# Optimization experiments

Hardware: AMD Instinct MI355X
Metric: run time of the kernel (lower is better)

## Reference

```python
import jax, jax.numpy as jnp
import numpy as np

K = 3; PAD = 1; CIN = 64; COUT = 64; B = 4; H = 128; W = 128


def setup_inputs() -> dict:
    key = jax.random.key(0)
    k1, k2, k3 = jax.random.split(key, 3)
    x = jax.random.normal(k1, (B, CIN, H, W), dtype=jnp.float32)
    # offset-predicting conv: [2*K*K, Cin, K, K]; small init -> sub-pixel offsets
    w_off = jax.random.normal(k2, (2 * K * K, CIN, K, K), dtype=jnp.float32) * 0.01
    b_off = jnp.zeros((2 * K * K,), dtype=jnp.float32)
    # deformable conv weight (bias=False): [Cout, Cin, K, K]
    w_def = jax.random.normal(k3, (COUT, CIN, K, K), dtype=jnp.float32) * 0.05
    return {"x": x, "w_off": w_off, "b_off": b_off, "w_def": w_def}


def _deform_conv(x, w_off, b_off, w_def):
    Bb, Cin, Hh, Ww = x.shape
    KK = K * K
    # 1) predict offsets with a regular 3x3 conv (stride 1, pad 1)
    off = jax.lax.conv_general_dilated(
        x, w_off, window_strides=(1, 1), padding=[(PAD, PAD), (PAD, PAD)],
        dimension_numbers=("NCHW", "OIHW", "NCHW"))
    off = off + b_off[None, :, None, None]          # [B, 2*KK, H, W]
    off = off.reshape(Bb, KK, 2, Hh, Ww)            # torchvision layout: (dy, dx) per tap
    dy, dx = off[:, :, 0], off[:, :, 1]             # [B, KK, H, W]

    # 2) sampling coordinates: p = p0 + p_k + offset
    ky = (jnp.arange(KK) // K).astype(x.dtype)
    kx = (jnp.arange(KK) % K).astype(x.dtype)
    hh = jnp.arange(Hh, dtype=x.dtype)
    ww = jnp.arange(Ww, dtype=x.dtype)
    py = hh[None, None, :, None] - PAD + ky[None, :, None, None] + dy   # [B,KK,H,W]
    px = ww[None, None, None, :] - PAD + kx[None, :, None, None] + dx

    # 3) bilinear sampling with zero padding outside the image
    y0f = jnp.floor(py); x0f = jnp.floor(px)
    fy = py - y0f; fx = px - x0f
    y0 = y0f.astype(jnp.int32); x0 = x0f.astype(jnp.int32)
    x_flat = x.reshape(Bb, Cin, Hh * Ww)

    def gather(yi, xi):
        valid = (yi >= 0) & (yi < Hh) & (xi >= 0) & (xi < Ww)
        idx = jnp.clip(yi, 0, Hh - 1) * Ww + jnp.clip(xi, 0, Ww - 1)     # [B,KK,H,W]
        g = jax.vmap(lambda xf, ix: xf[:, ix.reshape(-1)])(x_flat, idx)  # [B,Cin,KK*H*W]
        return g.reshape(Bb, Cin, KK, Hh, Ww) * valid[:, None].astype(x.dtype)

    sampled = (gather(y0, x0)         * ((1 - fy) * (1 - fx))[:, None]
             + gather(y0, x0 + 1)     * ((1 - fy) * fx)[:, None]
             + gather(y0 + 1, x0)     * (fy * (1 - fx))[:, None]
             + gather(y0 + 1, x0 + 1) * (fy * fx)[:, None])               # [B,Cin,KK,H,W]

    # 4) convolution accumulation over (Cin, kernel taps)
    return jnp.einsum('bckhw,ock->bohw', sampled, w_def.reshape(COUT, Cin, KK))


def reference(x, w_off, b_off, w_def):
    return _deform_conv(x, w_off, b_off, w_def)
```

## Files before the change

### kernel.cpp

```cpp
#include <hip/hip_runtime.h>
#include <hip/hip_fp16.h>

#define Bn   4
#define CINc 64
#define COUTc 64
#define Hn   128
#define Wn   128
#define HW   (Hn * Wn)
#define KKc  9
#define NOFF 18

typedef short bf16x8 __attribute__((ext_vector_type(8)));
typedef float f32x4  __attribute__((ext_vector_type(4)));
typedef float f32x2  __attribute__((ext_vector_type(2)));

__device__ inline unsigned short f2bf(float f) {
    unsigned int u = __float_as_uint(f);
    return (unsigned short)((u + 0x7fffu + ((u >> 16) & 1u)) >> 16);
}

__device__ inline void dma16(const void* g, void* l) {
#if __has_builtin(__builtin_amdgcn_global_load_lds)
    __builtin_amdgcn_global_load_lds(
        (__attribute__((address_space(1))) void*)(g),
        (__attribute__((address_space(3))) void*)(l), 16, 0, 0);
#else
    *(uint4*)l = *(const uint4*)g;
#endif
}

__global__ __launch_bounds__(256) void prep_all(
        const float* __restrict__ x, unsigned short* __restrict__ xt,
        const float* __restrict__ w_off, const float* __restrict__ w_def,
        unsigned short* __restrict__ wkb_sw, unsigned short* __restrict__ wob_sw) {
    int gb = blockIdx.x;
    int t  = threadIdx.x;
    if (gb < 1024) {
        __shared__ float s[64][65];
        int half = gb & 1;
        int h    = (gb >> 1) & 127;
        int b    = gb >> 8;
        int w0   = half * 64;
        int w = t & 63, cg = t >> 6;

        const float* xb = x + (size_t)b * CINc * HW + (size_t)h * Wn + w0 + w;
        #pragma unroll
        for (int i = 0; i < 16; ++i) {
            int c = cg * 16 + i;
            s[c][w] = xb[(size_t)c * HW];
        }
        __syncthreads();

        int cpair = t & 31, pxg = t >> 5;
        unsigned* xtp = (unsigned*)xt;
        #pragma unroll
        for (int i = 0; i < 8; ++i) {
            int px = pxg * 8 + i;
            float v0 = s[cpair * 2][px], v1 = s[cpair * 2 + 1][px];
            unsigned d = (unsigned)f2bf(v0) | ((unsigned)f2bf(v1) << 16);
            xtp[(((size_t)(b * Hn + h) * Wn) + w0 + px) * 32 + cpair] = d;
        }
        return;
    }
    int idx = (gb - 1024) * 256 + t;
    if (idx < 36864) {
        int j = idx & 7, l = (idx >> 3) & 63, s = idx >> 9;
        int k = s >> 3, kc = (s >> 2) & 1, ot = s & 3;
        int l15 = l & 15, quad = l >> 4;
        int o = ot * 16 + l15, c = kc * 32 + quad * 8 + j;
        wkb_sw[idx] = f2bf(w_def[((size_t)o * 64 + c) * 9 + k]);
    }
    int i2 = idx - 36864;
    if (i2 >= 0 && i2 < 18432) {
        int j = i2 & 7, l = (i2 >> 3) & 63, s = i2 >> 9;
        int tt = s >> 2, kc = (s >> 1) & 1, mt = s & 1;
        int l15 = l & 15, quad = l >> 4;
        int m = mt * 16 + l15, c = kc * 32 + quad * 8 + j;
        unsigned short v = 0;
        if (m < NOFF) v = f2bf(w_off[((size_t)m * 64 + c) * 9 + tt]);
        wob_sw[i2] = v;
    }
}


#define BFBUILD(C, kc, BF, W0, W1, W2, W3)                                   \
    do {                                                                     \
        const unsigned* t0 = (const unsigned*)&(C)[(kc) * 4 + 0];            \
        const unsigned* t1 = (const unsigned*)&(C)[(kc) * 4 + 1];            \
        const unsigned* b0 = (const unsigned*)&(C)[(kc) * 4 + 2];            \
        const unsigned* b1 = (const unsigned*)&(C)[(kc) * 4 + 3];            \
        _Pragma("unroll")                                                    \
        for (int jd = 0; jd < 4; ++jd) {                                     \
            f32x2 t0p = {__uint_as_float(t0[jd] << 16),                      \
                         __uint_as_float(t0[jd] & 0xFFFF0000u)};             \
            f32x2 t1p = {__uint_as_float(t1[jd] << 16),                      \
                         __uint_as_float(t1[jd] & 0xFFFF0000u)};             \
            f32x2 b0p = {__uint_as_float(b0[jd] << 16),                      \
                         __uint_as_float(b0[jd] & 0xFFFF0000u)};             \
            f32x2 b1p = {__uint_as_float(b1[jd] << 16),                      \
                         __uint_as_float(b1[jd] & 0xFFFF0000u)};             \
            f32x2 vv = t0p * (W0) + t1p * (W1) + b0p * (W2) + b1p * (W3);    \
            unsigned pk;                                                     \
            asm("v_cvt_pk_bf16_f32 %0, %1, %2"                               \
                : "=v"(pk) : "v"(vv.x), "v"(vv.y));                          \
            (BF).u[jd] = pk;                                                 \
        }                                                                    \
    } while (0)

#define TAP(k, SOFF)                                                         \
    do {                                                                     \
        const uint4* C = R[(k) & 1];                                         \
        union { unsigned u; __half2 hv; } c01, c23;                          \
        c01.u = pw01[(k)]; c23.u = pw23[(k)];                                \
        float W0 = __low2float(c01.hv), W1 = __high2float(c01.hv);           \
        float W2 = __low2float(c23.hv), W3 = __high2float(c23.hv);           \
        union { bf16x8 v; unsigned u[4]; } bfa, bfb;                         \
        BFBUILD(C, 0, bfa, W0, W1, W2, W3);                                  \
        BFBUILD(C, 1, bfb, W0, W1, W2, W3);                                  \
        _Pragma("unroll")                                                    \
        for (int ot = 0; ot < 4; ++ot) {                                     \
            bf16x8 af0 = s_w[(((k) * 2 + 0) * 4 + ot + (SOFF)) * 64 + lane]; \
            acc[ot] = __builtin_amdgcn_mfma_f32_16x16x32_bf16(               \
                af0, bfa.v, acc[ot], 0, 0, 0);                               \
            bf16x8 af1 = s_w[(((k) * 2 + 1) * 4 + ot + (SOFF)) * 64 + lane]; \
            acc[ot] = __builtin_amdgcn_mfma_f32_16x16x32_bf16(               \
                af1, bfb.v, acc[ot], 0, 0, 0);                               \
        }                                                                    \
    } while (0)

__global__ __launch_bounds__(512, 4) void fused_deform_v13(
        const unsigned short* __restrict__ xt,
        const unsigned short* __restrict__ wob_sw,
        const unsigned short* __restrict__ wkb_sw,
        const float* __restrict__ b_off, float* __restrict__ out) {
    __shared__ bf16x8 s_w[40 * 64];

    int gid  = blockIdx.x;
    int xcd  = gid & 7;
    int j    = gid >> 3;
    int hh   = j & 15;
    int b    = j >> 4;
    int h    = xcd * 16 + hh;
    int tid  = threadIdx.x;
    int lane = tid & 63;
    int wave = __builtin_amdgcn_readfirstlane(tid >> 6);
    int l15  = lane & 15;
    int quad = lane >> 4;
    int p    = wave * 16 + l15;

    #pragma unroll
    for (int i = 0; i < 5; ++i) {
        int seg = i * 8 + wave;
        if (seg < 36) {
            int ebase = seg * 64;
            dma16((const uint4*)wob_sw + ebase + lane,
                  (char*)s_w + (size_t)ebase * 16);
        }
    }

    uint4 L[9][2];
    unsigned msk[9];
    const unsigned short* xtb = xt + (size_t)b * HW * 64;
    #pragma unroll
    for (int t9 = 0; t9 < 9; ++t9) {
        int ty = t9 / 3, tx = t9 % 3;
        int y  = h - 1 + ty;
        int xg = p - 1 + tx;
        bool v = (y >= 0) && (y < Hn) && (xg >= 0) && (xg < Wn);
        msk[t9] = v ? 0xFFFFFFFFu : 0u;
        int yc = min(max(y, 0), Hn - 1);
        int xc = min(max(xg, 0), Wn - 1);
        size_t base = ((size_t)yc * Wn + xc) * 64;
        L[t9][0] = *(const uint4*)(xtb + base + quad * 8);
        L[t9][1] = *(const uint4*)(xtb + base + 32 + quad * 8);
    }
    __syncthreads();

    f32x4 oa0 = (f32x4){0.f, 0.f, 0.f, 0.f};
    f32x4 oa1 = (f32x4){0.f, 0.f, 0.f, 0.f};
    #pragma unroll
    for (int t9 = 0; t9 < 9; ++t9) {
        unsigned m = msk[t9];
        #pragma unroll
        for (int kc = 0; kc < 2; ++kc) {
            union { bf16x8 v; uint4 u; } bf;
            bf.u = L[t9][kc];
            bf.u.x &= m; bf.u.y &= m; bf.u.z &= m; bf.u.w &= m;
            bf16x8 a0 = s_w[((t9 * 2 + kc) * 2 + 0) * 64 + lane];
            bf16x8 a1 = s_w[((t9 * 2 + kc) * 2 + 1) * 64 + lane];
            oa0 = __builtin_amdgcn_mfma_f32_16x16x32_bf16(a0, bf.v, oa0, 0, 0, 0);
            oa1 = __builtin_amdgcn_mfma_f32_16x16x32_bf16(a1, bf.v, oa1, 0, 0, 0);
        }
    }

    unsigned my_ad[3]  = {0, 0, 0};
    unsigned my_w01[3] = {0, 0, 0};
    unsigned my_w23[3] = {0, 0, 0};
    auto phase1 = [&](int k, float dy, float dx, int slot) {
        float py  = (float)(h - 1 + k / 3) + dy;
        float pxf = (float)(p - 1 + k % 3) + dx;
        float y0f = floorf(py), x0f = floorf(pxf);
        float fy = py - y0f, fx = pxf - x0f;
        int y0 = (int)y0f, x0 = (int)x0f;
        bool vy0 = (y0 >= 0) & (y0 < Hn);
        bool vy1 = (y0 + 1 >= 0) & (y0 + 1 < Hn);
        bool vx0 = (x0 >= 0) & (x0 < Wn);
        bool vx1 = (x0 + 1 >= 0) & (x0 + 1 < Wn);
        float wy0 = vy0 ? 1.f - fy : 0.f;
        float wy1 = vy1 ? fy : 0.f;
        float wx0 = vx0 ? 1.f - fx : 0.f;
        float wx1 = vx1 ? fx : 0.f;
        int xc = min(max(x0, 0), Wn - 2);
        bool sel0 = (min(max(x0, 0), Wn - 1) != xc);
        bool sel1 = ((min(max(x0 + 1, 0), Wn - 1) - xc) == 1);
        float Wa = (sel0 ? 0.f : wx0) + (sel1 ? 0.f : wx1);
        float Wb = (sel0 ? wx0 : 0.f) + (sel1 ? wx1 : 0.f);
        int yc0 = min(max(y0, 0), Hn - 1), yc1 = min(max(y0 + 1, 0), Hn - 1);
        union { __half2 hv; unsigned u; } c01, c23;
        c01.hv = __floats2half2_rn(wy0 * Wa, wy0 * Wb);
        c23.hv = __floats2half2_rn(wy1 * Wa, wy1 * Wb);
        my_ad[slot]  = (unsigned)yc0 | ((unsigned)yc1 << 8) | ((unsigned)xc << 16);
        my_w01[slot] = c01.u;
        my_w23[slot] = c23.u;
    };
    int kb = quad * 2;
    phase1(kb,     oa0[0] + b_off[4 * quad],     oa0[1] + b_off[4 * quad + 1], 0);
    phase1(kb + 1, oa0[2] + b_off[4 * quad + 2], oa0[3] + b_off[4 * quad + 3], 1);
    if (quad == 0)
        phase1(8, oa1[0] + b_off[16], oa1[1] + b_off[17], 2);
    __syncthreads();

    #pragma unroll
    for (int i = 0; i < 4; ++i) {
        int seg = i * 8 + wave;
        dma16((const uint4*)wkb_sw + (size_t)seg * 64 + lane,
              (char*)s_w + (size_t)seg * 1024);
    }

    unsigned at[KKc], ab[KKc];
    unsigned pw01[KKc], pw23[KKc];
    #pragma unroll
    for (int k = 0; k < KKc; ++k) {
        int src  = (k < 8) ? ((k >> 1) * 16 + l15) : l15;
        int slot = (k < 8) ? (k & 1) : 2;
        unsigned ad  = (unsigned)__shfl((int)my_ad[slot],  src, 64);
        pw01[k] = (unsigned)__shfl((int)my_w01[slot], src, 64);
        pw23[k] = (unsigned)__shfl((int)my_w23[slot], src, 64);
        int xc = (int)(ad >> 16);
        at[k] = (unsigned)(((ad & 255u) * Wn + xc) * 64);
        ab[k] = (unsigned)((((ad >> 8) & 255u) * Wn + xc) * 64);
    }
    __syncthreads();

    f32x4 acc[4];
    #pragma unroll
    for (int ot = 0; ot < 4; ++ot) acc[ot] = (f32x4){0.f, 0.f, 0.f, 0.f};

    uint4 R[2][8];
    int co0 = quad * 8, co1 = 32 + quad * 8;

    #define FETCH(kk, st)                                            \
        do {                                                         \
            R[st][0] = *(const uint4*)(xtb + at[kk] + co0);          \
            R[st][1] = *(const uint4*)(xtb + at[kk] + 64 + co0);     \
            R[st][2] = *(const uint4*)(xtb + ab[kk] + co0);          \
            R[st][3] = *(const uint4*)(xtb + ab[kk] + 64 + co0);     \
            R[st][4] = *(const uint4*)(xtb + at[kk] + co1);          \
            R[st][5] = *(const uint4*)(xtb + at[kk] + 64 + co1);     \
            R[st][6] = *(const uint4*)(xtb + ab[kk] + co1);          \
            R[st][7] = *(const uint4*)(xtb + ab[kk] + 64 + co1);     \
        } while (0)

    FETCH(0, 0);
    FETCH(1, 1); TAP(0, 0);
    FETCH(2, 0); TAP(1, 0);
    FETCH(3, 1); TAP(2, 0);
    FETCH(4, 0); TAP(3, 0);
    __syncthreads();

    #pragma unroll
    for (int i = 0; i < 5; ++i) {
        int seg = i * 8 + wave;
        dma16((const uint4*)wkb_sw + (size_t)(32 + seg) * 64 + lane,
              (char*)s_w + (size_t)seg * 1024);
    }

    union { bf16x8 v; unsigned u[4]; } bf40, bf41;
    {
        const uint4* C = R[0];
        union { unsigned u; __half2 hv; } c01, c23;
        c01.u = pw01[4]; c23.u = pw23[4];
        float W0 = __low2float(c01.hv), W1 = __high2float(c01.hv);
        float W2 = __low2float(c23.hv), W3 = __high2float(c23.hv);
        BFBUILD(C, 0, bf40, W0, W1, W2, W3);
        BFBUILD(C, 1, bf41, W0, W1, W2, W3);
    }
    FETCH(5, 1);
    __syncthreads();

    #pragma unroll
    for (int ot = 0; ot < 4; ++ot) {
        bf16x8 af0 = s_w[(0 + ot) * 64 + lane];
        acc[ot] = __builtin_amdgcn_mfma_f32_16x16x32_bf16(af0, bf40.v, acc[ot], 0, 0, 0);
        bf16x8 af1 = s_w[(4 + ot) * 64 + lane];
        acc[ot] = __builtin_amdgcn_mfma_f32_16x16x32_bf16(af1, bf41.v, acc[ot], 0, 0, 0);
    }

    FETCH(6, 0); TAP(5, -32);
    FETCH(7, 1); TAP(6, -32);
    FETCH(8, 0); TAP(7, -32);
    TAP(8, -32);
    #undef FETCH

    #pragma unroll
    for (int ot = 0; ot < 4; ++ot)
        #pragma unroll
        for (int r = 0; r < 4; ++r) {
            int o = ot * 16 + quad * 4 + r;
            out[(((size_t)b * COUTc + o) * Hn + h) * Wn + p] = acc[ot][r];
        }
}

extern "C" void kernel_launch(void* const* d_in, const int* in_sizes, int n_in,
                              void* d_out, int out_size, void* d_ws, size_t ws_size,
                              hipStream_t stream) {
    const float* x     = (const float*)d_in[0];
    const float* w_off = (const float*)d_in[1];
    const float* b_off = (const float*)d_in[2];
    const float* w_def = (const float*)d_in[3];
    float* out = (float*)d_out;

    char* ws = (char*)d_ws;
    unsigned short* xt = (unsigned short*)ws;
    ws += (size_t)Bn * HW * CINc * sizeof(unsigned short);
    unsigned short* wkb_sw = (unsigned short*)ws;
    ws += 36864 * sizeof(unsigned short);
    unsigned short* wob_sw = (unsigned short*)ws;

    prep_all<<<1024 + 216, 256, 0, stream>>>(x, xt, w_off, w_def, wkb_sw, wob_sw);
    fused_deform_v13<<<Bn * Hn, 512, 0, stream>>>(xt, wob_sw, wkb_sw, b_off, out);
}
```

Before: 115.5 us.

## Split fused deform kernel into offset kernel and half-row gather/MFMA kernel

Splits the fused kernel into two launches. The first predicts the offsets and writes per-pixel, per-tap sampling records (address and fp16 bilinear weights) to workspace. The second reads those records back and does the gather and MFMA accumulation, using 256-thread blocks over half a row so it launches twice as many blocks. This aims to raise parallelism and occupancy for the gather/MFMA phase. The cost is an extra launch and a round trip of about 7 MB of records through global memory.

```diff
diff --git a/kernel.cpp b/kernel.cpp
--- a/kernel.cpp
+++ b/kernel.cpp
@@ -128,12 +128,29 @@
         }                                                                    \
     } while (0)
 
-__global__ __launch_bounds__(512, 4) void fused_deform_v13(
+#define FETCH(kk, st)                                                \
+    do {                                                             \
+        unsigned ad_ = ad[kk];                                       \
+        unsigned xc_ = ad_ >> 16;                                    \
+        unsigned at_ = (((ad_ & 255u) << 7) + xc_) << 6;             \
+        unsigned ab_ = ((((ad_ >> 8) & 255u) << 7) + xc_) << 6;      \
+        R[st][0] = *(const uint4*)(xtb + at_ + co0);                 \
+        R[st][1] = *(const uint4*)(xtb + at_ + 64 + co0);            \
+        R[st][2] = *(const uint4*)(xtb + ab_ + co0);                 \
+        R[st][3] = *(const uint4*)(xtb + ab_ + 64 + co0);            \
+        R[st][4] = *(const uint4*)(xtb + at_ + co1);                 \
+        R[st][5] = *(const uint4*)(xtb + at_ + 64 + co1);            \
+        R[st][6] = *(const uint4*)(xtb + ab_ + co1);                 \
+        R[st][7] = *(const uint4*)(xtb + ab_ + 64 + co1);            \
+    } while (0)
+
+__global__ __launch_bounds__(512, 4) void offs_k(
         const unsigned short* __restrict__ xt,
         const unsigned short* __restrict__ wob_sw,
-        const unsigned short* __restrict__ wkb_sw,
-        const float* __restrict__ b_off, float* __restrict__ out) {
-    __shared__ bf16x8 s_w[40 * 64];
+        const float* __restrict__ b_off,
+        unsigned* __restrict__ rec_ad, unsigned* __restrict__ rec_w01,
+        unsigned* __restrict__ rec_w23) {
+    __shared__ bf16x8 s_w[36 * 64];
 
     int gid  = blockIdx.x;
     int xcd  = gid & 7;
@@ -228,27 +245,58 @@
     phase1(kb + 1, oa0[2] + b_off[4 * quad + 2], oa0[3] + b_off[4 * quad + 3], 1);
     if (quad == 0)
         phase1(8, oa1[0] + b_off[16], oa1[1] + b_off[17], 2);
-    __syncthreads();
-
-    #pragma unroll
-    for (int i = 0; i < 4; ++i) {
-        int seg = i * 8 + wave;
+
+    int rb = ((b * Hn + h) * KKc) * Wn + p;
+    rec_ad [rb + kb * Wn]       = my_ad[0];
+    rec_w01[rb + kb * Wn]       = my_w01[0];
+    rec_w23[rb + kb * Wn]       = my_w23[0];
+    rec_ad [rb + (kb + 1) * Wn] = my_ad[1];
+    rec_w01[rb + (kb + 1) * Wn] = my_w01[1];
+    rec_w23[rb + (kb + 1) * Wn] = my_w23[1];
+    if (quad == 0) {
+        rec_ad [rb + 8 * Wn] = my_ad[2];
+        rec_w01[rb + 8 * Wn] = my_w01[2];
+        rec_w23[rb + 8 * Wn] = my_w23[2];
+    }
+}
+
+__global__ __launch_bounds__(256, 4) void gmain(
+        const unsigned short* __restrict__ xt,
+        const unsigned short* __restrict__ wkb_sw,
+        const unsigned* __restrict__ rec_ad, const unsigned* __restrict__ rec_w01,
+        const unsigned* __restrict__ rec_w23, float* __restrict__ out) {
+    __shared__ bf16x8 s_w[40 * 64];
+
+    int gid  = blockIdx.x;
+    int xcd  = gid & 7;
+    int t2   = gid >> 3;
+    int wh   = t2 & 1;
+    int jj   = t2 >> 1;
+    int hh   = jj & 15;
+    int b    = jj >> 4;
+    int h    = xcd * 16 + hh;
+    int tid  = threadIdx.x;
+    int lane = tid & 63;
+    int wave = __builtin_amdgcn_readfirstlane(tid >> 6);
+    int l15  = lane & 15;
+    int quad = lane >> 4;
+    int p    = wh * 64 + wave * 16 + l15;
+
+    #pragma unroll
+    for (int i = 0; i < 8; ++i) {
+        int seg = i * 4 + wave;
         dma16((const uint4*)wkb_sw + (size_t)seg * 64 + lane,
               (char*)s_w + (size_t)seg * 1024);
     }
 
-    unsigned at[KKc], ab[KKc];
-    unsigned pw01[KKc], pw23[KKc];
+    const unsigned short* xtb = xt + (size_t)b * HW * 64;
+    unsigned ad[KKc], pw01[KKc], pw23[KKc];
+    int rb = ((b * Hn + h) * KKc) * Wn + p;
     #pragma unroll
     for (int k = 0; k < KKc; ++k) {
-        int src  = (k < 8) ? ((k >> 1) * 16 + l15) : l15;
-        int slot = (k < 8) ? (k & 1) : 2;
-        unsigned ad  = (unsigned)__shfl((int)my_ad[slot],  src, 64);
-        pw01[k] = (unsigned)__shfl((int)my_w01[slot], src, 64);
-        pw23[k] = (unsigned)__shfl((int)my_w23[slot], src, 64);
-        int xc = (int)(ad >> 16);
-        at[k] = (unsigned)(((ad & 255u) * Wn + xc) * 64);
-        ab[k] = (unsigned)((((ad >> 8) & 255u) * Wn + xc) * 64);
+        ad[k]   = rec_ad [rb + k * Wn];
+        pw01[k] = rec_w01[rb + k * Wn];
+        pw23[k] = rec_w23[rb + k * Wn];
     }
     __syncthreads();
 
@@ -258,18 +306,6 @@
 
     uint4 R[2][8];
     int co0 = quad * 8, co1 = 32 + quad * 8;
-
-    #define FETCH(kk, st)                                            \
-        do {                                                         \
-            R[st][0] = *(const uint4*)(xtb + at[kk] + co0);          \
-            R[st][1] = *(const uint4*)(xtb + at[kk] + 64 + co0);     \
-            R[st][2] = *(const uint4*)(xtb + ab[kk] + co0);          \
-            R[st][3] = *(const uint4*)(xtb + ab[kk] + 64 + co0);     \
-            R[st][4] = *(const uint4*)(xtb + at[kk] + co1);          \
-            R[st][5] = *(const uint4*)(xtb + at[kk] + 64 + co1);     \
-            R[st][6] = *(const uint4*)(xtb + ab[kk] + co1);          \
-            R[st][7] = *(const uint4*)(xtb + ab[kk] + 64 + co1);     \
-        } while (0)
 
     FETCH(0, 0);
     FETCH(1, 1); TAP(0, 0);
@@ -279,8 +315,8 @@
     __syncthreads();
 
     #pragma unroll
-    for (int i = 0; i < 5; ++i) {
-        int seg = i * 8 + wave;
+    for (int i = 0; i < 10; ++i) {
+        int seg = i * 4 + wave;
         dma16((const uint4*)wkb_sw + (size_t)(32 + seg) * 64 + lane,
               (char*)s_w + (size_t)seg * 1024);
     }
@@ -310,7 +346,6 @@
     FETCH(7, 1); TAP(6, -32);
     FETCH(8, 0); TAP(7, -32);
     TAP(8, -32);
-    #undef FETCH
 
     #pragma unroll
     for (int ot = 0; ot < 4; ++ot)
@@ -336,7 +371,14 @@
     unsigned short* wkb_sw = (unsigned short*)ws;
     ws += 36864 * sizeof(unsigned short);
     unsigned short* wob_sw = (unsigned short*)ws;
+    ws += 36864;
+    unsigned* rec_ad = (unsigned*)ws;
+    ws += (size_t)Bn * Hn * KKc * Wn * 4;
+    unsigned* rec_w01 = (unsigned*)ws;
+    ws += (size_t)Bn * Hn * KKc * Wn * 4;
+    unsigned* rec_w23 = (unsigned*)ws;
 
     prep_all<<<1024 + 216, 256, 0, stream>>>(x, xt, w_off, w_def, wkb_sw, wob_sw);
-    fused_deform_v13<<<Bn * Hn, 512, 0, stream>>>(xt, wob_sw, wkb_sw, b_off, out);
-}
+    offs_k<<<Bn * Hn, 512, 0, stream>>>(xt, wob_sw, b_off, rec_ad, rec_w01, rec_w23);
+    gmain<<<Bn * Hn * 2, 256, 0, stream>>>(xt, wkb_sw, rec_ad, rec_w01, rec_w23, out);
+}
```

New measurement: 120.9 us. 4.7% more time.

## Split each row across two 256-thread blocks and vectorize the prep transpose loads

Applied to the files above, without the earlier changes.

The fused kernel now launches twice as many blocks with 256 threads each, each block covering half an image row. Shared memory for the weight tiles shrinks to 36 segments, so the deform-weight staging is restructured into three DMA phases, with tap 8 handled in its own phase. The per-tap address arithmetic is recomputed inside FETCH from packed coordinates rather than held in precomputed arrays, which lowers register pressure. The prep transpose now reads x with float4 loads. The aim is better occupancy and load balance, at the cost of more block launches, extra barriers and every block reloading the offset weights.

```diff
diff --git a/kernel.cpp b/kernel.cpp
--- a/kernel.cpp
+++ b/kernel.cpp
@@ -41,13 +41,17 @@
         int h    = (gb >> 1) & 127;
         int b    = gb >> 8;
         int w0   = half * 64;
-        int w = t & 63, cg = t >> 6;
-
-        const float* xb = x + (size_t)b * CINc * HW + (size_t)h * Wn + w0 + w;
+
+        const float* xb = x + (size_t)b * CINc * HW + (size_t)h * Wn + w0;
+        int c0 = t >> 4, wq = (t & 15) * 4;
         #pragma unroll
-        for (int i = 0; i < 16; ++i) {
-            int c = cg * 16 + i;
-            s[c][w] = xb[(size_t)c * HW];
+        for (int i = 0; i < 4; ++i) {
+            int c = c0 + i * 16;
+            float4 v = *(const float4*)(xb + (size_t)c * HW + wq);
+            s[c][wq]     = v.x;
+            s[c][wq + 1] = v.y;
+            s[c][wq + 2] = v.z;
+            s[c][wq + 3] = v.w;
         }
         __syncthreads();
 
@@ -128,16 +132,34 @@
         }                                                                    \
     } while (0)
 
-__global__ __launch_bounds__(512, 4) void fused_deform_v13(
+#define FETCH(kk, st)                                                \
+    do {                                                             \
+        unsigned ad_ = ad[kk];                                       \
+        unsigned xc_ = ad_ >> 16;                                    \
+        unsigned at_ = (((ad_ & 255u) << 7) + xc_) << 6;             \
+        unsigned ab_ = ((((ad_ >> 8) & 255u) << 7) + xc_) << 6;      \
+        R[st][0] = *(const uint4*)(xtb + at_ + co0);                 \
+        R[st][1] = *(const uint4*)(xtb + at_ + 64 + co0);            \
+        R[st][2] = *(const uint4*)(xtb + ab_ + co0);                 \
+        R[st][3] = *(const uint4*)(xtb + ab_ + 64 + co0);            \
+        R[st][4] = *(const uint4*)(xtb + at_ + co1);                 \
+        R[st][5] = *(const uint4*)(xtb + at_ + 64 + co1);            \
+        R[st][6] = *(const uint4*)(xtb + ab_ + co1);                 \
+        R[st][7] = *(const uint4*)(xtb + ab_ + 64 + co1);            \
+    } while (0)
+
+__global__ __launch_bounds__(256, 4) void fused_deform_v18(
         const unsigned short* __restrict__ xt,
         const unsigned short* __restrict__ wob_sw,
         const unsigned short* __restrict__ wkb_sw,
         const float* __restrict__ b_off, float* __restrict__ out) {
-    __shared__ bf16x8 s_w[40 * 64];
+    __shared__ bf16x8 s_w[36 * 64];
 
     int gid  = blockIdx.x;
     int xcd  = gid & 7;
-    int j    = gid >> 3;
+    int r    = gid >> 3;
+    int wh   = r & 1;
+    int j    = r >> 1;
     int hh   = j & 15;
     int b    = j >> 4;
     int h    = xcd * 16 + hh;
@@ -146,16 +168,14 @@
     int wave = __builtin_amdgcn_readfirstlane(tid >> 6);
     int l15  = lane & 15;
     int quad = lane >> 4;
-    int p    = wave * 16 + l15;
-
-    #pragma unroll
-    for (int i = 0; i < 5; ++i) {
-        int seg = i * 8 + wave;
-        if (seg < 36) {
-            int ebase = seg * 64;
-            dma16((const uint4*)wob_sw + ebase + lane,
-                  (char*)s_w + (size_t)ebase * 16);
-        }
+    int p    = wh * 64 + wave * 16 + l15;
+
+    #pragma unroll
+    for (int i = 0; i < 9; ++i) {
+        int seg = i * 4 + wave;
+        int ebase = seg * 64;
+        dma16((const uint4*)wob_sw + ebase + lane,
+              (char*)s_w + (size_t)ebase * 16);
     }
 
     uint4 L[9][2];
@@ -231,24 +251,20 @@
     __syncthreads();
 
     #pragma unroll
-    for (int i = 0; i < 4; ++i) {
-        int seg = i * 8 + wave;
+    for (int i = 0; i < 8; ++i) {
+        int seg = i * 4 + wave;
         dma16((const uint4*)wkb_sw + (size_t)seg * 64 + lane,
               (char*)s_w + (size_t)seg * 1024);
     }
 
-    unsigned at[KKc], ab[KKc];
-    unsigned pw01[KKc], pw23[KKc];
+    unsigned ad[KKc], pw01[KKc], pw23[KKc];
     #pragma unroll
     for (int k = 0; k < KKc; ++k) {
         int src  = (k < 8) ? ((k >> 1) * 16 + l15) : l15;
         int slot = (k < 8) ? (k & 1) : 2;
-        unsigned ad  = (unsigned)__shfl((int)my_ad[slot],  src, 64);
+        ad[k]   = (unsigned)__shfl((int)my_ad[slot],  src, 64);
         pw01[k] = (unsigned)__shfl((int)my_w01[slot], src, 64);
         pw23[k] = (unsigned)__shfl((int)my_w23[slot], src, 64);
-        int xc = (int)(ad >> 16);
-        at[k] = (unsigned)(((ad & 255u) * Wn + xc) * 64);
-        ab[k] = (unsigned)((((ad >> 8) & 255u) * Wn + xc) * 64);
     }
     __syncthreads();
 
@@ -258,18 +274,6 @@
 
     uint4 R[2][8];
     int co0 = quad * 8, co1 = 32 + quad * 8;
-
-    #define FETCH(kk, st)                                            \
-        do {                                                         \
-            R[st][0] = *(const uint4*)(xtb + at[kk] + co0);          \
-            R[st][1] = *(const uint4*)(xtb + at[kk] + 64 + co0);     \
-            R[st][2] = *(const uint4*)(xtb + ab[kk] + co0);          \
-            R[st][3] = *(const uint4*)(xtb + ab[kk] + 64 + co0);     \
-            R[st][4] = *(const uint4*)(xtb + at[kk] + co1);          \
-            R[st][5] = *(const uint4*)(xtb + at[kk] + 64 + co1);     \
-            R[st][6] = *(const uint4*)(xtb + ab[kk] + co1);          \
-            R[st][7] = *(const uint4*)(xtb + ab[kk] + 64 + co1);     \
-        } while (0)
 
     FETCH(0, 0);
     FETCH(1, 1); TAP(0, 0);
@@ -279,8 +283,8 @@
     __syncthreads();
 
     #pragma unroll
-    for (int i = 0; i < 5; ++i) {
-        int seg = i * 8 + wave;
+    for (int i = 0; i < 8; ++i) {
+        int seg = i * 4 + wave;
         dma16((const uint4*)wkb_sw + (size_t)(32 + seg) * 64 + lane,
               (char*)s_w + (size_t)seg * 1024);
     }
@@ -309,15 +313,41 @@
     FETCH(6, 0); TAP(5, -32);
     FETCH(7, 1); TAP(6, -32);
     FETCH(8, 0); TAP(7, -32);
-    TAP(8, -32);
-    #undef FETCH
+    __syncthreads();
+
+    #pragma unroll
+    for (int i = 0; i < 2; ++i) {
+        int seg = i * 4 + wave;
+        dma16((const uint4*)wkb_sw + (size_t)(64 + seg) * 64 + lane,
+              (char*)s_w + (size_t)seg * 1024);
+    }
+
+    union { bf16x8 v; unsigned u[4]; } bf80, bf81;
+    {
+        const uint4* C = R[0];
+        union { unsigned u; __half2 hv; } c01, c23;
+        c01.u = pw01[8]; c23.u = pw23[8];
+        float W0 = __low2float(c01.hv), W1 = __high2float(c01.hv);
+        float W2 = __low2float(c23.hv), W3 = __high2float(c23.hv);
+        BFBUILD(C, 0, bf80, W0, W1, W2, W3);
+        BFBUILD(C, 1, bf81, W0, W1, W2, W3);
+    }
+    __syncthreads();
+
+    #pragma unroll
+    for (int ot = 0; ot < 4; ++ot) {
+        bf16x8 af0 = s_w[(0 + ot) * 64 + lane];
+        acc[ot] = __builtin_amdgcn_mfma_f32_16x16x32_bf16(af0, bf80.v, acc[ot], 0, 0, 0);
+        bf16x8 af1 = s_w[(4 + ot) * 64 + lane];
+        acc[ot] = __builtin_amdgcn_mfma_f32_16x16x32_bf16(af1, bf81.v, acc[ot], 0, 0, 0);
+    }
 
     #pragma unroll
     for (int ot = 0; ot < 4; ++ot)
         #pragma unroll
-        for (int r = 0; r < 4; ++r) {
-            int o = ot * 16 + quad * 4 + r;
-            out[(((size_t)b * COUTc + o) * Hn + h) * Wn + p] = acc[ot][r];
+        for (int rr = 0; rr < 4; ++rr) {
+            int o = ot * 16 + quad * 4 + rr;
+            out[(((size_t)b * COUTc + o) * Hn + h) * Wn + p] = acc[ot][rr];
         }
 }
 
@@ -338,5 +368,5 @@
     unsigned short* wob_sw = (unsigned short*)ws;
 
     prep_all<<<1024 + 216, 256, 0, stream>>>(x, xt, w_off, w_def, wkb_sw, wob_sw);
-    fused_deform_v13<<<Bn * Hn, 512, 0, stream>>>(xt, wob_sw, wkb_sw, b_off, out);
-}
+    fused_deform_v18<<<Bn * Hn * 2, 256, 0, stream>>>(xt, wob_sw, wkb_sw, b_off, out);
+}
```

New measurement: 116.9 us. About the same (+1.3%).
